# Kernel tuning notes

Measured on AMD Instinct MI355X. Metric: run time of the kernel, lower is better.

Reference implementation:

```python
import jax, jax.numpy as jnp
import numpy as np

N_HEAD = 8
D_MODEL = 512
D_K = 64
D_V = 64
LN_EPS = 1e-6


def setup_inputs() -> dict:
    key = jax.random.key(0)
    ks = jax.random.split(key, 8)
    B, L = 4, 1024
    inp = {
        "q": jax.random.normal(ks[0], (B, L, D_MODEL), dtype=jnp.float32),
        "k": jax.random.normal(ks[1], (B, L, D_MODEL), dtype=jnp.float32),
        "v": jax.random.normal(ks[2], (B, L, D_MODEL), dtype=jnp.float32),
        "w_qs": jax.random.normal(ks[3], (D_MODEL, N_HEAD * D_K), dtype=jnp.float32) * 0.02,
        "w_ks": jax.random.normal(ks[4], (D_MODEL, N_HEAD * D_K), dtype=jnp.float32) * 0.02,
        "w_vs": jax.random.normal(ks[5], (D_MODEL, N_HEAD * D_V), dtype=jnp.float32) * 0.02,
        "w_sk": jax.random.normal(ks[6], (D_V, N_HEAD * D_V), dtype=jnp.float32) * 0.02,
        "w_fc": jax.random.normal(ks[7], (D_V, D_MODEL), dtype=jnp.float32) * 0.02,
        "ln_gamma": jnp.ones((D_MODEL,), dtype=jnp.float32),
        "ln_beta": jnp.zeros((D_MODEL,), dtype=jnp.float32),
    }
    return inp


def reference(q, k, v, w_qs, w_ks, w_vs, w_sk, w_fc, ln_gamma, ln_beta):
    B, Lq, _ = q.shape
    Lk = k.shape[1]
    temp = jnp.asarray(D_K ** 0.5, q.dtype)
    residual = q

    # QKV projections (bias=False), split heads: [B, H, L, d]
    qh = (q @ w_qs).reshape(B, Lq, N_HEAD, D_K).transpose(0, 2, 1, 3)
    kh = (k @ w_ks).reshape(B, Lk, N_HEAD, D_K).transpose(0, 2, 1, 3)
    vh = (v @ w_vs).reshape(B, Lk, N_HEAD, D_V).transpose(0, 2, 1, 3)

    # scaled dot-product attention (dropout in eval mode = identity)
    attn = jax.nn.softmax(jnp.einsum('bhqd,bhkd->bhqk', qh / temp, kh), axis=-1)
    o = jnp.einsum('bhqk,bhkd->bhqd', attn, vh)  # [B, H, Lq, D_V]

    # SPA: selective parallel attention head gating
    u = o.sum(axis=1)                       # [B, Lq, D_V]
    s = u.mean(axis=1)                      # adaptive avg pool over Lq -> [B, D_V]
    g = jax.nn.softmax((s @ w_sk).reshape(B, N_HEAD, D_V), axis=1)  # softmax over heads
    f = o * g[:, :, None, :]                # gate each head, broadcast over Lq
    qo = f.sum(axis=1)                      # sum heads -> [B, Lq, D_V]

    # fc + residual + LayerNorm (dropout eval = identity)
    out = qo @ w_fc + residual              # [B, Lq, D_MODEL]
    mu = out.mean(axis=-1, keepdims=True)
    var = out.var(axis=-1, keepdims=True)
    out = (out - mu) * jax.lax.rsqrt(var + LN_EPS) * ln_gamma + ln_beta
    return out, attn
```

## Files before the change

### kernel.cpp

```cpp
#include <hip/hip_runtime.h>
#include <hip/hip_bf16.h>
#include <cstdint>

#define NH 8
#define DM 512
#define DH 64
#define NB 4
#define SL 1024

typedef __attribute__((ext_vector_type(8))) short bf16x8;
typedef __attribute__((ext_vector_type(4))) float f32x4;

static __device__ __forceinline__ float bf2f(short s) {
  union { unsigned int u; float f; } c;
  c.u = ((unsigned int)(unsigned short)s) << 16;
  return c.f;
}
static __device__ __forceinline__ unsigned short f2bfbits(float f) {
  union { float f; unsigned int u; } c; c.f = f;
  unsigned int lsb = (c.u >> 16) & 1u;
  unsigned int r = c.u + 0x7fffu + lsb;
  return (unsigned short)(r >> 16);
}

__global__ __launch_bounds__(256) void k_cvt_act(
    const float* __restrict__ q, const float* __restrict__ k, const float* __restrict__ v,
    ushort* __restrict__ qb, ushort* __restrict__ kb, ushort* __restrict__ vb) {
  int i = blockIdx.x * 256 + threadIdx.x;
  {
    float4 f = ((const float4*)q)[i];
    ushort4 r = { f2bfbits(f.x), f2bfbits(f.y), f2bfbits(f.z), f2bfbits(f.w) };
    *(ushort4*)(qb + 4 * i) = r;
  }
  {
    float4 f = ((const float4*)k)[i];
    ushort4 r = { f2bfbits(f.x), f2bfbits(f.y), f2bfbits(f.z), f2bfbits(f.w) };
    *(ushort4*)(kb + 4 * i) = r;
  }
  {
    float4 f = ((const float4*)v)[i];
    ushort4 r = { f2bfbits(f.x), f2bfbits(f.y), f2bfbits(f.z), f2bfbits(f.w) };
    *(ushort4*)(vb + 4 * i) = r;
  }
}

__global__ __launch_bounds__(256) void k_cvt_wT(
    const float* __restrict__ w0, const float* __restrict__ w1, const float* __restrict__ w2,
    ushort* __restrict__ o0, ushort* __restrict__ o1, ushort* __restrict__ o2) {
  __shared__ ushort tile[64][65];
  const float* src = blockIdx.z == 0 ? w0 : (blockIdx.z == 1 ? w1 : w2);
  ushort* dst = blockIdx.z == 0 ? o0 : (blockIdx.z == 1 ? o1 : o2);
  int k0 = blockIdx.x * 64, n0 = blockIdx.y * 64;
  int t = threadIdx.x;
  #pragma unroll
  for (int i = 0; i < 16; ++i) {
    int lin = t + i * 256, r = lin >> 6, c = lin & 63;
    tile[r][c] = f2bfbits(src[(size_t)(k0 + r) * DM + n0 + c]);
  }
  __syncthreads();
  #pragma unroll
  for (int i = 0; i < 16; ++i) {
    int lin = t + i * 256, r = lin >> 6, c = lin & 63;
    dst[(size_t)(n0 + r) * DM + k0 + c] = tile[c][r];
  }
}

__global__ __launch_bounds__(256) void k_cvt_wfc(const float* __restrict__ w, ushort* __restrict__ o) {
  int i = blockIdx.x * 256 + threadIdx.x;
  float4 f = ((const float4*)w)[i];
  ushort4 r = { f2bfbits(f.x), f2bfbits(f.y), f2bfbits(f.z), f2bfbits(f.w) };
  *(ushort4*)(o + 4 * i) = r;
}

__global__ __launch_bounds__(256) void k_proj(
    const ushort* __restrict__ qb, const ushort* __restrict__ kb, const ushort* __restrict__ vb,
    const ushort* __restrict__ wqT, const ushort* __restrict__ wkT, const ushort* __restrict__ wvT,
    ushort* __restrict__ Qh, ushort* __restrict__ Kh, ushort* __restrict__ VhT) {
  int z = blockIdx.z;
  const ushort* A = z == 0 ? qb : (z == 1 ? kb : vb);
  const ushort* W = z == 0 ? wqT : (z == 1 ? wkT : wvT);
  ushort* Out = z == 0 ? Qh : (z == 1 ? Kh : VhT);
  float scale = z == 0 ? 0.125f : 1.0f;

  int wid = threadIdx.x >> 6, l = threadIdx.x & 63;
  int lr = l & 15, lg = l >> 4;
  int row0 = blockIdx.x * 64 + wid * 16;
  int col0 = blockIdx.y * 64;
  const ushort* Arow = A + (size_t)(row0 + lr) * DM + lg * 8;

  f32x4 acc0 = {0.f, 0.f, 0.f, 0.f}, acc1 = acc0, acc2 = acc0, acc3 = acc0;
  #pragma unroll 4
  for (int kt = 0; kt < 16; ++kt) {
    bf16x8 a = *(const bf16x8*)(Arow + kt * 32);
    bf16x8 b0 = *(const bf16x8*)(W + (size_t)(col0 + 0 * 16 + lr) * DM + kt * 32 + lg * 8);
    bf16x8 b1 = *(const bf16x8*)(W + (size_t)(col0 + 1 * 16 + lr) * DM + kt * 32 + lg * 8);
    bf16x8 b2 = *(const bf16x8*)(W + (size_t)(col0 + 2 * 16 + lr) * DM + kt * 32 + lg * 8);
    bf16x8 b3 = *(const bf16x8*)(W + (size_t)(col0 + 3 * 16 + lr) * DM + kt * 32 + lg * 8);
    acc0 = __builtin_amdgcn_mfma_f32_16x16x32_bf16(a, b0, acc0, 0, 0, 0);
    acc1 = __builtin_amdgcn_mfma_f32_16x16x32_bf16(a, b1, acc1, 0, 0, 0);
    acc2 = __builtin_amdgcn_mfma_f32_16x16x32_bf16(a, b2, acc2, 0, 0, 0);
    acc3 = __builtin_amdgcn_mfma_f32_16x16x32_bf16(a, b3, acc3, 0, 0, 0);
  }
  f32x4 accs[4] = {acc0, acc1, acc2, acc3};
  #pragma unroll
  for (int ct = 0; ct < 4; ++ct) {
    int gcol = col0 + ct * 16 + lr;
    int h = gcol >> 6, d = gcol & 63;
    #pragma unroll
    for (int r = 0; r < 4; ++r) {
      int grow = row0 + lg * 4 + r;
      int bb = grow >> 10, li = grow & 1023;
      float val = accs[ct][r] * scale;
      size_t addr;
      if (z == 2) addr = ((size_t)((bb * NH + h) * DH + d)) * SL + li;
      else        addr = ((size_t)((bb * NH + h) * SL + li)) * DH + d;
      Out[addr] = f2bfbits(val);
    }
  }
}

__global__ __launch_bounds__(256) void k_attn(
    const ushort* __restrict__ Qh, const ushort* __restrict__ Kh, const ushort* __restrict__ VhT,
    float* __restrict__ attn_out, float* __restrict__ O) {
  __shared__ __align__(16) float S[16][1028];
  __shared__ __align__(16) ushort P[16][1032];

  int rt = blockIdx.x, h = blockIdx.y, bb = blockIdx.z;
  int bh = bb * NH + h;
  int wid = threadIdx.x >> 6, l = threadIdx.x & 63;
  int lr = l & 15, lg = l >> 4;

  const ushort* Qbase = Qh + ((size_t)(bh * SL + rt * 16 + lr)) * DH + lg * 8;
  bf16x8 aQ0 = *(const bf16x8*)(Qbase);
  bf16x8 aQ1 = *(const bf16x8*)(Qbase + 32);
  const ushort* Kbase = Kh + (size_t)bh * SL * DH;

  #pragma unroll 4
  for (int ct = 0; ct < 16; ++ct) {
    int col0 = wid * 256 + ct * 16;
    const ushort* kp = Kbase + (size_t)(col0 + lr) * DH + lg * 8;
    bf16x8 b0 = *(const bf16x8*)(kp);
    bf16x8 b1 = *(const bf16x8*)(kp + 32);
    f32x4 acc = {0.f, 0.f, 0.f, 0.f};
    acc = __builtin_amdgcn_mfma_f32_16x16x32_bf16(aQ0, b0, acc, 0, 0, 0);
    acc = __builtin_amdgcn_mfma_f32_16x16x32_bf16(aQ1, b1, acc, 0, 0, 0);
    #pragma unroll
    for (int r = 0; r < 4; ++r) S[lg * 4 + r][col0 + lr] = acc[r];
  }
  __syncthreads();

  size_t attn_base = ((size_t)(bh * SL + rt * 16)) * SL;
  #pragma unroll
  for (int rr = 0; rr < 4; ++rr) {
    int r = wid * 4 + rr;
    float vv[16];
    float m = -1e30f;
    #pragma unroll
    for (int i = 0; i < 16; ++i) { vv[i] = S[r][l + 64 * i]; m = fmaxf(m, vv[i]); }
    #pragma unroll
    for (int o = 32; o; o >>= 1) m = fmaxf(m, __shfl_xor(m, o));
    float s = 0.f;
    #pragma unroll
    for (int i = 0; i < 16; ++i) { vv[i] = __expf(vv[i] - m); s += vv[i]; }
    #pragma unroll
    for (int o = 32; o; o >>= 1) s += __shfl_xor(s, o);
    float inv = 1.0f / s;
    float* arow = attn_out + attn_base + (size_t)r * SL;
    #pragma unroll
    for (int i = 0; i < 16; ++i) {
      float p = vv[i] * inv;
      arow[l + 64 * i] = p;
      P[r][l + 64 * i] = f2bfbits(p);
    }
  }
  __syncthreads();

  const ushort* Vbase = VhT + (size_t)bh * DH * SL + (size_t)(wid * 16 + lr) * SL + lg * 8;
  f32x4 acc = {0.f, 0.f, 0.f, 0.f};
  #pragma unroll 8
  for (int kt = 0; kt < 32; ++kt) {
    bf16x8 aP = *(const bf16x8*)(&P[lr][kt * 32 + lg * 8]);
    bf16x8 bV = *(const bf16x8*)(Vbase + kt * 32);
    acc = __builtin_amdgcn_mfma_f32_16x16x32_bf16(aP, bV, acc, 0, 0, 0);
  }
  #pragma unroll
  for (int r = 0; r < 4; ++r)
    O[((size_t)(bh * SL + rt * 16 + lg * 4 + r)) * DH + wid * 16 + lr] = acc[r];
}

__global__ __launch_bounds__(256) void k_reduce(const float* __restrict__ O, float* __restrict__ partial) {
  int slab = blockIdx.x, bb = blockIdx.y;
  int d = threadIdx.x & 63, sub = threadIdx.x >> 6;
  float s = 0.f;
  for (int h = 0; h < NH; ++h) {
    const float* base = O + ((size_t)((bb * NH + h) * SL + slab * 32 + sub * 8)) * DH + d;
    #pragma unroll
    for (int li = 0; li < 8; ++li) s += base[(size_t)li * DH];
  }
  __shared__ float red[4][64];
  red[sub][d] = s;
  __syncthreads();
  if (threadIdx.x < 64) {
    float t = red[0][d] + red[1][d] + red[2][d] + red[3][d];
    partial[(bb * 32 + slab) * 64 + d] = t;
  }
}

__global__ __launch_bounds__(256) void k_gate(const float* __restrict__ partial,
                                              const float* __restrict__ wsk, float* __restrict__ g) {
  int bb = blockIdx.x;
  int t = threadIdx.x;
  __shared__ float red[4][64];
  __shared__ float sl[64];
  __shared__ float logit[512];
  int d = t & 63, q4 = t >> 6;
  float s = 0.f;
  for (int i = 0; i < 8; ++i) s += partial[(bb * 32 + q4 * 8 + i) * 64 + d];
  red[q4][d] = s;
  __syncthreads();
  if (t < 64) sl[t] = (red[0][t] + red[1][t] + red[2][t] + red[3][t]) * (1.0f / 1024.0f);
  __syncthreads();
  #pragma unroll
  for (int jj = 0; jj < 2; ++jj) {
    int j = t + jj * 256;
    float lg = 0.f;
    #pragma unroll 8
    for (int c = 0; c < 64; ++c) lg += sl[c] * wsk[c * DM + j];
    logit[j] = lg;
  }
  __syncthreads();
  if (t < 64) {
    float m = -1e30f;
    #pragma unroll
    for (int h = 0; h < NH; ++h) m = fmaxf(m, logit[h * 64 + t]);
    float sum = 0.f, e[NH];
    #pragma unroll
    for (int h = 0; h < NH; ++h) { e[h] = __expf(logit[h * 64 + t] - m); sum += e[h]; }
    float inv = 1.0f / sum;
    #pragma unroll
    for (int h = 0; h < NH; ++h) g[bb * DM + h * 64 + t] = e[h] * inv;
  }
}

__global__ __launch_bounds__(256) void k_final(
    const float* __restrict__ O, const float* __restrict__ g, const ushort* __restrict__ wfc,
    const float* __restrict__ q, const float* __restrict__ gamma, const float* __restrict__ beta,
    float* __restrict__ out) {
  __shared__ __align__(16) ushort wl[32768];
  __shared__ __align__(16) float qo[16][64];
  __shared__ __align__(16) float gl[512];
  int lt = blockIdx.x, bb = blockIdx.y;
  int t = threadIdx.x;

  gl[t] = g[bb * DM + t];
  gl[t + 256] = g[bb * DM + 256 + t];
  {
    int jg2 = t & 15, hi = t >> 4;
    #pragma unroll
    for (int m = 0; m < 16; ++m) {
      int di = m * 16 + hi;
      int d = di >> 2, i8 = di & 3;
      bf16x8 w8 = *(const bf16x8*)(wfc + d * DM + jg2 * 32 + i8 * 8);
      *(bf16x8*)(wl + (size_t)(d * 64 + i8 * 16 + jg2) * 8) = w8;
    }
  }
  __syncthreads();

  int r = t >> 4, jg = t & 15;
  int l = lt * 16 + r;
  {
    float4 acc; acc.x = acc.y = acc.z = acc.w = 0.f;
    #pragma unroll
    for (int h = 0; h < NH; ++h) {
      float4 ov = *(const float4*)(O + ((size_t)((bb * NH + h) * SL + l)) * DH + jg * 4);
      float4 gv = *(const float4*)(gl + h * 64 + jg * 4);
      acc.x += ov.x * gv.x; acc.y += ov.y * gv.y; acc.z += ov.z * gv.z; acc.w += ov.w * gv.w;
    }
    *(float4*)&qo[r][jg * 4] = acc;
  }
  __syncthreads();

  float val[32];
  const float* qrow = q + ((size_t)(bb * SL + l)) * DM + jg * 32;
  #pragma unroll
  for (int i4 = 0; i4 < 8; ++i4) *(float4*)&val[i4 * 4] = *(const float4*)(qrow + i4 * 4);

  for (int d = 0; d < 64; ++d) {
    float qd = qo[r][d];
    #pragma unroll
    for (int i8 = 0; i8 < 4; ++i8) {
      bf16x8 wv8 = *(const bf16x8*)(wl + (size_t)(d * 64 + i8 * 16 + jg) * 8);
      #pragma unroll
      for (int e = 0; e < 8; ++e) val[i8 * 8 + e] += qd * bf2f(wv8[e]);
    }
  }

  float s = 0.f, ss = 0.f;
  #pragma unroll
  for (int i = 0; i < 32; ++i) { s += val[i]; ss += val[i] * val[i]; }
  #pragma unroll
  for (int m = 1; m < 16; m <<= 1) { s += __shfl_xor(s, m, 16); ss += __shfl_xor(ss, m, 16); }
  float mu = s * (1.0f / 512.0f);
  float var = ss * (1.0f / 512.0f) - mu * mu;
  float rstd = rsqrtf(var + 1e-6f);

  float* orow = out + ((size_t)(bb * SL + l)) * DM + jg * 32;
  const float* gam = gamma + jg * 32;
  const float* bet = beta + jg * 32;
  #pragma unroll
  for (int i = 0; i < 32; ++i)
    orow[i] = (val[i] - mu) * rstd * gam[i] + bet[i];
}

extern "C" void kernel_launch(void* const* d_in, const int* in_sizes, int n_in,
                              void* d_out, int out_size, void* d_ws, size_t ws_size,
                              hipStream_t stream) {
  (void)in_sizes; (void)n_in; (void)out_size; (void)ws_size;
  const float* q     = (const float*)d_in[0];
  const float* k     = (const float*)d_in[1];
  const float* v     = (const float*)d_in[2];
  const float* w_qs  = (const float*)d_in[3];
  const float* w_ks  = (const float*)d_in[4];
  const float* w_vs  = (const float*)d_in[5];
  const float* w_sk  = (const float*)d_in[6];
  const float* w_fc  = (const float*)d_in[7];
  const float* gamma = (const float*)d_in[8];
  const float* beta  = (const float*)d_in[9];

  float* out  = (float*)d_out;
  float* attn = out + (size_t)NB * SL * DM;

  char* wsb = (char*)d_ws;
  ushort* qb   = (ushort*)(wsb + 0);
  ushort* kb   = (ushort*)(wsb + 4194304);
  ushort* vb   = (ushort*)(wsb + 8388608);
  ushort* wqT  = (ushort*)(wsb + 12582912);
  ushort* wkT  = (ushort*)(wsb + 13107200);
  ushort* wvT  = (ushort*)(wsb + 13631488);
  ushort* wfcb = (ushort*)(wsb + 14155776);
  ushort* Qh   = (ushort*)(wsb + 14221312);
  ushort* Kh   = (ushort*)(wsb + 18415616);
  ushort* VhT  = (ushort*)(wsb + 22609920);
  float*  O    = (float*)(wsb + 26804224);
  float*  part = (float*)(wsb + 35192832);
  float*  gbuf = (float*)(wsb + 35225600);

  k_cvt_act<<<dim3(2048), dim3(256), 0, stream>>>(q, k, v, qb, kb, vb);
  k_cvt_wT<<<dim3(8, 8, 3), dim3(256), 0, stream>>>(w_qs, w_ks, w_vs, wqT, wkT, wvT);
  k_cvt_wfc<<<dim3(32), dim3(256), 0, stream>>>(w_fc, wfcb);
  k_proj<<<dim3(64, 8, 3), dim3(256), 0, stream>>>(qb, kb, vb, wqT, wkT, wvT, Qh, Kh, VhT);
  k_attn<<<dim3(64, 8, 4), dim3(256), 0, stream>>>(Qh, Kh, VhT, attn, O);
  k_reduce<<<dim3(32, 4), dim3(256), 0, stream>>>(O, part);
  k_gate<<<dim3(4), dim3(256), 0, stream>>>(part, w_sk, gbuf);
  k_final<<<dim3(64, 4), dim3(256), 0, stream>>>(O, gbuf, wfcb, q, gamma, beta, out);
}
```

Before: 196.7 us.

## Shrink attention LDS to one swizzled bf16 buffer and fuse row max

Replaces the fp32 score tile plus the separate bf16 probability tile with a single bf16 buffer, XOR-swizzled to avoid bank conflicts, that is reused in place for probabilities. Per-row maxima are computed during the QK MFMA loop and reduced through a small shared array, removing the separate max pass. It also adds a launch-bounds occupancy hint. This cuts LDS per block from roughly 98KB to 32KB so more blocks fit per CU, at the cost of rounding scores to bf16 before the softmax, which lowers accuracy of the fp32 attn output.

Result: faster. 169.1 us (-14.1%).

```diff
diff --git a/kernel.cpp b/kernel.cpp
--- a/kernel.cpp
+++ b/kernel.cpp
@@ -119,22 +119,24 @@
   }
 }
 
-__global__ __launch_bounds__(256) void k_attn(
+__global__ __launch_bounds__(256, 4) void k_attn(
     const ushort* __restrict__ Qh, const ushort* __restrict__ Kh, const ushort* __restrict__ VhT,
     float* __restrict__ attn_out, float* __restrict__ O) {
-  __shared__ __align__(16) float S[16][1028];
-  __shared__ __align__(16) ushort P[16][1032];
+  __shared__ __align__(16) ushort Sl[16 * 1024];
+  __shared__ float wmax[4][16];
 
   int rt = blockIdx.x, h = blockIdx.y, bb = blockIdx.z;
   int bh = bb * NH + h;
   int wid = threadIdx.x >> 6, l = threadIdx.x & 63;
   int lr = l & 15, lg = l >> 4;
+  char* Sb = (char*)Sl;
 
   const ushort* Qbase = Qh + ((size_t)(bh * SL + rt * 16 + lr)) * DH + lg * 8;
   bf16x8 aQ0 = *(const bf16x8*)(Qbase);
   bf16x8 aQ1 = *(const bf16x8*)(Qbase + 32);
   const ushort* Kbase = Kh + (size_t)bh * SL * DH;
 
+  float mloc[4] = {-1e30f, -1e30f, -1e30f, -1e30f};
   #pragma unroll 4
   for (int ct = 0; ct < 16; ++ct) {
     int col0 = wid * 256 + ct * 16;
@@ -145,7 +147,21 @@
     acc = __builtin_amdgcn_mfma_f32_16x16x32_bf16(aQ0, b0, acc, 0, 0, 0);
     acc = __builtin_amdgcn_mfma_f32_16x16x32_bf16(aQ1, b1, acc, 0, 0, 0);
     #pragma unroll
-    for (int r = 0; r < 4; ++r) S[lg * 4 + r][col0 + lr] = acc[r];
+    for (int r = 0; r < 4; ++r) {
+      int row = lg * 4 + r;
+      ushort us = f2bfbits(acc[r]);
+      *(ushort*)(Sb + (((row << 11) + ((col0 + lr) << 1)) ^ ((row & 7) << 4))) = us;
+      mloc[r] = fmaxf(mloc[r], bf2f(us));
+    }
+  }
+  #pragma unroll
+  for (int r = 0; r < 4; ++r) {
+    float m = mloc[r];
+    m = fmaxf(m, __shfl_xor(m, 1));
+    m = fmaxf(m, __shfl_xor(m, 2));
+    m = fmaxf(m, __shfl_xor(m, 4));
+    m = fmaxf(m, __shfl_xor(m, 8));
+    if (lr == 0) wmax[wid][lg * 4 + r] = m;
   }
   __syncthreads();
 
@@ -153,24 +169,23 @@
   #pragma unroll
   for (int rr = 0; rr < 4; ++rr) {
     int r = wid * 4 + rr;
-    float vv[16];
-    float m = -1e30f;
-    #pragma unroll
-    for (int i = 0; i < 16; ++i) { vv[i] = S[r][l + 64 * i]; m = fmaxf(m, vv[i]); }
-    #pragma unroll
-    for (int o = 32; o; o >>= 1) m = fmaxf(m, __shfl_xor(m, o));
+    float M = fmaxf(fmaxf(wmax[0][r], wmax[1][r]), fmaxf(wmax[2][r], wmax[3][r]));
+    float e[16];
     float s = 0.f;
     #pragma unroll
-    for (int i = 0; i < 16; ++i) { vv[i] = __expf(vv[i] - m); s += vv[i]; }
+    for (int i = 0; i < 16; ++i) {
+      float v = bf2f(*(ushort*)(Sb + (((r << 11) + ((l + 64 * i) << 1)) ^ ((r & 7) << 4))));
+      e[i] = __expf(v - M); s += e[i];
+    }
     #pragma unroll
     for (int o = 32; o; o >>= 1) s += __shfl_xor(s, o);
     float inv = 1.0f / s;
     float* arow = attn_out + attn_base + (size_t)r * SL;
     #pragma unroll
     for (int i = 0; i < 16; ++i) {
-      float p = vv[i] * inv;
+      float p = e[i] * inv;
       arow[l + 64 * i] = p;
-      P[r][l + 64 * i] = f2bfbits(p);
+      *(ushort*)(Sb + (((r << 11) + ((l + 64 * i) << 1)) ^ ((r & 7) << 4))) = f2bfbits(p);
     }
   }
   __syncthreads();
@@ -179,7 +194,7 @@
   f32x4 acc = {0.f, 0.f, 0.f, 0.f};
   #pragma unroll 8
   for (int kt = 0; kt < 32; ++kt) {
-    bf16x8 aP = *(const bf16x8*)(&P[lr][kt * 32 + lg * 8]);
+    bf16x8 aP = *(const bf16x8*)(Sb + (((lr << 11) + ((kt * 32 + lg * 8) << 1)) ^ ((lr & 7) << 4)));
     bf16x8 bV = *(const bf16x8*)(Vbase + kt * 32);
     acc = __builtin_amdgcn_mfma_f32_16x16x32_bf16(aP, bV, acc, 0, 0, 0);
   }
```

## Restructure attention kernel into two-pass online softmax with per-wave query tiles

Applied to the files above, without the earlier changes.

Rewrites k_attn so that each wave owns a 16-row query tile. A first pass over K computes the running max and sum with an online softmax in the exp2 domain, with log2(e) folded into the Q projection scale. A second pass recomputes QK^T, writes normalized probabilities directly to global memory, and feeds bf16-packed P through a small per-wave LDS tile into the PV MFMAs. This removes the large shared-memory S/P buffers and the block barriers, and adds XCD-aware block remapping and occupancy hints. The cost is computing QK^T twice.

Measured after the change: 194.6 us. About the same (-1.1%).

```diff
diff --git a/kernel.cpp b/kernel.cpp
--- a/kernel.cpp
+++ b/kernel.cpp
@@ -10,6 +10,7 @@
 
 typedef __attribute__((ext_vector_type(8))) short bf16x8;
 typedef __attribute__((ext_vector_type(4))) float f32x4;
+typedef __attribute__((ext_vector_type(4))) unsigned int u32x4;
 
 static __device__ __forceinline__ float bf2f(short s) {
   union { unsigned int u; float f; } c;
@@ -80,7 +81,7 @@
   const ushort* A = z == 0 ? qb : (z == 1 ? kb : vb);
   const ushort* W = z == 0 ? wqT : (z == 1 ? wkT : wvT);
   ushort* Out = z == 0 ? Qh : (z == 1 ? Kh : VhT);
-  float scale = z == 0 ? 0.125f : 1.0f;
+  float scale = z == 0 ? 0.125f * 1.44269504088896f : 1.0f;
 
   int wid = threadIdx.x >> 6, l = threadIdx.x & 63;
   int lr = l & 15, lg = l >> 4;
@@ -119,73 +120,95 @@
   }
 }
 
-__global__ __launch_bounds__(256) void k_attn(
+__global__ __launch_bounds__(256, 2) void k_attn(
     const ushort* __restrict__ Qh, const ushort* __restrict__ Kh, const ushort* __restrict__ VhT,
     float* __restrict__ attn_out, float* __restrict__ O) {
-  __shared__ __align__(16) float S[16][1028];
-  __shared__ __align__(16) ushort P[16][1032];
-
-  int rt = blockIdx.x, h = blockIdx.y, bb = blockIdx.z;
-  int bh = bb * NH + h;
+  __shared__ __align__(16) unsigned int Plds[4][16 * 20];
+
+  int bid = blockIdx.x;
+  int xcd = bid & 7;
+  int loc = bid >> 3;
+  int bh  = xcd * 4 + (loc >> 4);
   int wid = threadIdx.x >> 6, l = threadIdx.x & 63;
-  int lr = l & 15, lg = l >> 4;
-
-  const ushort* Qbase = Qh + ((size_t)(bh * SL + rt * 16 + lr)) * DH + lg * 8;
-  bf16x8 aQ0 = *(const bf16x8*)(Qbase);
-  bf16x8 aQ1 = *(const bf16x8*)(Qbase + 32);
-  const ushort* Kbase = Kh + (size_t)bh * SL * DH;
-
+  int rt  = (loc & 15) * 4 + wid;
+  int lr = l & 15, g = l >> 4;
+  int q0 = rt * 16;
+
+  const ushort* Qbase = Qh + ((size_t)(bh * SL + q0 + lr)) * DH + g * 8;
+  bf16x8 bQ0 = *(const bf16x8*)(Qbase);
+  bf16x8 bQ1 = *(const bf16x8*)(Qbase + 32);
+  const ushort* Kbase = Kh + (size_t)bh * SL * DH + (size_t)lr * DH + g * 8;
+
+  float m = -1e30f, s = 0.f;
   #pragma unroll 4
-  for (int ct = 0; ct < 16; ++ct) {
-    int col0 = wid * 256 + ct * 16;
-    const ushort* kp = Kbase + (size_t)(col0 + lr) * DH + lg * 8;
-    bf16x8 b0 = *(const bf16x8*)(kp);
-    bf16x8 b1 = *(const bf16x8*)(kp + 32);
+  for (int kc = 0; kc < 64; ++kc) {
+    const ushort* kp = Kbase + (size_t)(kc * 16) * DH;
+    bf16x8 a0 = *(const bf16x8*)(kp);
+    bf16x8 a1 = *(const bf16x8*)(kp + 32);
     f32x4 acc = {0.f, 0.f, 0.f, 0.f};
-    acc = __builtin_amdgcn_mfma_f32_16x16x32_bf16(aQ0, b0, acc, 0, 0, 0);
-    acc = __builtin_amdgcn_mfma_f32_16x16x32_bf16(aQ1, b1, acc, 0, 0, 0);
-    #pragma unroll
-    for (int r = 0; r < 4; ++r) S[lg * 4 + r][col0 + lr] = acc[r];
-  }
-  __syncthreads();
-
-  size_t attn_base = ((size_t)(bh * SL + rt * 16)) * SL;
-  #pragma unroll
-  for (int rr = 0; rr < 4; ++rr) {
-    int r = wid * 4 + rr;
-    float vv[16];
-    float m = -1e30f;
-    #pragma unroll
-    for (int i = 0; i < 16; ++i) { vv[i] = S[r][l + 64 * i]; m = fmaxf(m, vv[i]); }
-    #pragma unroll
-    for (int o = 32; o; o >>= 1) m = fmaxf(m, __shfl_xor(m, o));
-    float s = 0.f;
-    #pragma unroll
-    for (int i = 0; i < 16; ++i) { vv[i] = __expf(vv[i] - m); s += vv[i]; }
-    #pragma unroll
-    for (int o = 32; o; o >>= 1) s += __shfl_xor(s, o);
-    float inv = 1.0f / s;
-    float* arow = attn_out + attn_base + (size_t)r * SL;
-    #pragma unroll
-    for (int i = 0; i < 16; ++i) {
-      float p = vv[i] * inv;
-      arow[l + 64 * i] = p;
-      P[r][l + 64 * i] = f2bfbits(p);
-    }
-  }
-  __syncthreads();
-
-  const ushort* Vbase = VhT + (size_t)bh * DH * SL + (size_t)(wid * 16 + lr) * SL + lg * 8;
-  f32x4 acc = {0.f, 0.f, 0.f, 0.f};
-  #pragma unroll 8
-  for (int kt = 0; kt < 32; ++kt) {
-    bf16x8 aP = *(const bf16x8*)(&P[lr][kt * 32 + lg * 8]);
-    bf16x8 bV = *(const bf16x8*)(Vbase + kt * 32);
-    acc = __builtin_amdgcn_mfma_f32_16x16x32_bf16(aP, bV, acc, 0, 0, 0);
-  }
-  #pragma unroll
-  for (int r = 0; r < 4; ++r)
-    O[((size_t)(bh * SL + rt * 16 + lg * 4 + r)) * DH + wid * 16 + lr] = acc[r];
+    acc = __builtin_amdgcn_mfma_f32_16x16x32_bf16(a0, bQ0, acc, 0, 0, 0);
+    acc = __builtin_amdgcn_mfma_f32_16x16x32_bf16(a1, bQ1, acc, 0, 0, 0);
+    float cm = fmaxf(fmaxf(acc[0], acc[1]), fmaxf(acc[2], acc[3]));
+    float mn = fmaxf(m, cm);
+    s = s * exp2f(m - mn)
+      + exp2f(acc[0] - mn) + exp2f(acc[1] - mn)
+      + exp2f(acc[2] - mn) + exp2f(acc[3] - mn);
+    m = mn;
+  }
+  {
+    float mo = __shfl_xor(m, 16), so = __shfl_xor(s, 16);
+    float mn = fmaxf(m, mo);
+    s = s * exp2f(m - mn) + so * exp2f(mo - mn); m = mn;
+    mo = __shfl_xor(m, 32); so = __shfl_xor(s, 32);
+    mn = fmaxf(m, mo);
+    s = s * exp2f(m - mn) + so * exp2f(mo - mn); m = mn;
+  }
+  const float M = m, inv = 1.0f / s;
+
+  float* attnrow = attn_out + (size_t)bh * SL * SL + (size_t)(q0 + lr) * SL;
+  const ushort* Vbase = VhT + (size_t)bh * DH * SL;
+  unsigned int* Pw = &Plds[wid][0];
+  f32x4 o0 = {0.f, 0.f, 0.f, 0.f}, o1 = o0, o2 = o0, o3 = o0;
+
+  #pragma unroll 2
+  for (int kb = 0; kb < 32; ++kb) {
+    #pragma unroll
+    for (int c = 0; c < 2; ++c) {
+      int k0 = kb * 32 + c * 16;
+      const ushort* kp = Kbase + (size_t)k0 * DH;
+      bf16x8 a0 = *(const bf16x8*)(kp);
+      bf16x8 a1 = *(const bf16x8*)(kp + 32);
+      f32x4 acc = {0.f, 0.f, 0.f, 0.f};
+      acc = __builtin_amdgcn_mfma_f32_16x16x32_bf16(a0, bQ0, acc, 0, 0, 0);
+      acc = __builtin_amdgcn_mfma_f32_16x16x32_bf16(a1, bQ1, acc, 0, 0, 0);
+      float p0 = exp2f(acc[0] - M) * inv;
+      float p1 = exp2f(acc[1] - M) * inv;
+      float p2 = exp2f(acc[2] - M) * inv;
+      float p3 = exp2f(acc[3] - M) * inv;
+      float4 pv = { p0, p1, p2, p3 };
+      *(float4*)(attnrow + k0 + 4 * g) = pv;
+      unsigned int pk0, pk1;
+      asm("v_cvt_pk_bf16_f32 %0, %1, %2" : "=v"(pk0) : "v"(p0), "v"(p1));
+      asm("v_cvt_pk_bf16_f32 %0, %1, %2" : "=v"(pk1) : "v"(p2), "v"(p3));
+      uint2 w2 = { pk0, pk1 };
+      *(uint2*)(Pw + lr * 20 + c * 8 + 2 * g) = w2;
+    }
+    union { u32x4 u; bf16x8 b; } ap;
+    ap.u = *(u32x4*)(Pw + lr * 20 + 4 * g);
+    #pragma unroll
+    for (int dt = 0; dt < 4; ++dt) {
+      bf16x8 bV = *(const bf16x8*)(Vbase + (size_t)(dt * 16 + lr) * SL + kb * 32 + g * 8);
+      f32x4& oo = dt == 0 ? o0 : (dt == 1 ? o1 : (dt == 2 ? o2 : o3));
+      oo = __builtin_amdgcn_mfma_f32_16x16x32_bf16(ap.b, bV, oo, 0, 0, 0);
+    }
+  }
+
+  f32x4 os[4] = { o0, o1, o2, o3 };
+  #pragma unroll
+  for (int dt = 0; dt < 4; ++dt)
+    #pragma unroll
+    for (int r = 0; r < 4; ++r)
+      O[((size_t)(bh * SL + q0 + 4 * g + r)) * DH + dt * 16 + lr] = os[dt][r];
 }
 
 __global__ __launch_bounds__(256) void k_reduce(const float* __restrict__ O, float* __restrict__ partial) {
@@ -349,7 +372,7 @@
   k_cvt_wT<<<dim3(8, 8, 3), dim3(256), 0, stream>>>(w_qs, w_ks, w_vs, wqT, wkT, wvT);
   k_cvt_wfc<<<dim3(32), dim3(256), 0, stream>>>(w_fc, wfcb);
   k_proj<<<dim3(64, 8, 3), dim3(256), 0, stream>>>(qb, kb, vb, wqT, wkT, wvT, Qh, Kh, VhT);
-  k_attn<<<dim3(64, 8, 4), dim3(256), 0, stream>>>(Qh, Kh, VhT, attn, O);
+  k_attn<<<dim3(512), dim3(256), 0, stream>>>(Qh, Kh, VhT, attn, O);
   k_reduce<<<dim3(32, 4), dim3(256), 0, stream>>>(O, part);
   k_gate<<<dim3(4), dim3(256), 0, stream>>>(part, w_sk, gbuf);
   k_final<<<dim3(64, 4), dim3(256), 0, stream>>>(O, gbuf, wfcb, q, gamma, beta, out);
```
